# Performance work log

Measured on AMD Instinct MI355X. Metric: run time of the kernel, lower is better.

The kernel has to match this reference:

```python
import jax, jax.numpy as jnp
import numpy as np

GRAPH_RADIUS = 0.125  # gcn_cfg['graph_radius']
N, D = 4096, 256      # num samples in batch, desc_len


def setup_inputs() -> dict:
    key = jax.random.key(0)
    k1, k2, k3, k4, k5, k6 = jax.random.split(key, 6)
    centers = jax.random.uniform(k1, (N, 3), dtype=jnp.float32)  # points in unit cube
    descriptors = jax.random.normal(k2, (N, D), dtype=jnp.float32)
    # EdgeConv MLPs: torch nn.Linear(2*D, D) -> weight [D, 2*D], bias [D]
    W1 = jax.random.normal(k3, (D, 2 * D), dtype=jnp.float32) * 0.05
    b1 = jax.random.normal(k4, (D,), dtype=jnp.float32) * 0.05
    W2 = jax.random.normal(k5, (D, 2 * D), dtype=jnp.float32) * 0.05
    b2 = jax.random.normal(k6, (D,), dtype=jnp.float32) * 0.05
    return {"centers": centers, "descriptors": descriptors,
            "W1": W1, "b1": b1, "W2": W2, "b2": b2}


def reference(centers, descriptors, W1, b1, W2, b2):
    # N star graphs: graph a has edges a->k for all k != a with ||c_k - c_a|| <= r.
    # Each node k in graph a receives at most ONE message (from anchor a); the
    # anchor receives none. EdgeConv(aggr='mean') message at target i from source j
    # is mlp(cat([x_i, x_j - x_i])); mean over a single message is the message.
    n = centers.shape[0]
    d = descriptors.shape[1]
    # pairwise squared distances [N, N]
    diff = centers[:, None, :] - centers[None, :, :]
    d2 = jnp.sum(diff * diff, axis=-1)
    mask = (d2 <= GRAPH_RADIUS * GRAPH_RADIUS) & (~jnp.eye(n, dtype=bool))
    M = mask.astype(descriptors.dtype)            # M[a, k]: k is neighbor of anchor a
    deg = jnp.sum(M, axis=1, keepdims=True)       # [N, 1] neighbors per anchor

    # conv1: h1[a, k] = M[a,k] * ( cat([x_k, x_a - x_k]) @ W1^T + b1 )
    #                 = M[a,k] * ( u[k] + v[a] + b1 )
    W1a, W1b = W1[:, :d], W1[:, d:]
    u = descriptors @ (W1a - W1b).T               # target-side term  [N, D]
    v = descriptors @ W1b.T                       # anchor-side term  [N, D]

    # conv2: anchor feature h1[a, a] = 0, so message = cat([h1, -h1]) @ W2^T + b2
    #        h2[a, k] = M[a,k] * ( h1[a,k] @ (W2a - W2b)^T + b2 )
    C = (W2[:, :d] - W2[:, d:]).T                 # [D, D]

    # global_mean_pool over the N nodes of each graph a:
    # pooled[a] = (1/N) * [ (sum_k M[a,k] u[k] + deg_a*(v[a]+b1)) @ C + deg_a*b2 ]
    Mu = M @ u                                    # [N, D]
    pooled = ((Mu + deg * (v + b1)) @ C + deg * b2) / n

    return jnp.concatenate([descriptors, pooled], axis=1)  # [N, 2D]
```

## Files before the change

### kernel.cpp

```cpp
#include <hip/hip_runtime.h>

#define NPTS 4096
#define DDIM 256
#define R2V 0.015625f
#define MAXDEG 512
#define NI 4

typedef __bf16 v8bf __attribute__((ext_vector_type(8)));
typedef float v4f __attribute__((ext_vector_type(4)));
typedef unsigned short ushort_t;

static __device__ __forceinline__ float bf2f(ushort_t s) {
    union { unsigned u; float f; } w; w.u = ((unsigned)s) << 16; return w.f;
}
static __device__ __forceinline__ ushort_t f2bf(float x) {
    return __builtin_bit_cast(ushort_t, (__bf16)x);
}

__global__ void prepEFt_kernel(const float* __restrict__ W1, const float* __restrict__ W2,
                               const float* __restrict__ b1, const float* __restrict__ b2,
                               ushort_t* __restrict__ EFt, float* __restrict__ g) {
    __shared__ float cs[4][256];
    __shared__ float b1s[256];
    int l0 = blockIdx.x * 4;
    int m = threadIdx.x;
    b1s[m] = b1[m];
#pragma unroll
    for (int q = 0; q < 4; ++q)
        cs[q][m] = W2[(l0 + q) * 512 + m] - W2[(l0 + q) * 512 + 256 + m];
    __syncthreads();
    float ae[4] = {0, 0, 0, 0}, af[4] = {0, 0, 0, 0}, ag[4] = {0, 0, 0, 0};
#pragma unroll 4
    for (int k = 0; k < 256; ++k) {
        float w1a = W1[k * 512 + m];
        float w1b = W1[k * 512 + 256 + m];
        float bk = b1s[k];
#pragma unroll
        for (int q = 0; q < 4; ++q) {
            float c = cs[q][k];
            ae[q] = fmaf(w1a - w1b, c, ae[q]);
            af[q] = fmaf(w1b, c, af[q]);
            ag[q] = fmaf(bk, c, ag[q]);
        }
    }
#pragma unroll
    for (int q = 0; q < 4; ++q) {
        EFt[(l0 + q) * 256 + m] = f2bf(ae[q]);
        EFt[(256 + l0 + q) * 256 + m] = f2bf(af[q]);
        if (m == 0) g[l0 + q] = ag[q] + b2[l0 + q];
    }
}

#define BM 64
#define BN 128
__launch_bounds__(256, 1)
__global__ void gemm_kernel(const float* __restrict__ desc, const ushort_t* __restrict__ EFt,
                            ushort_t* __restrict__ PQ) {
    __shared__ ushort_t Asm[BM * 256];
    __shared__ ushort_t Bsm[BN * 256];
    int tid = threadIdx.x;
    int i0 = blockIdx.x * BM;
    int n0 = blockIdx.y * BN;
    const float* gA = desc + i0 * 256;
#pragma unroll
    for (int c = 0; c < 8; ++c) {
        int u = c * 256 + tid;
        int fb = u * 16;
        int row = fb >> 9, colb = fb & 511;
        float4 f0 = *(const float4*)(gA + u * 8);
        float4 f1 = *(const float4*)(gA + u * 8 + 4);
        ushort_t h[8];
        h[0] = f2bf(f0.x); h[1] = f2bf(f0.y); h[2] = f2bf(f0.z); h[3] = f2bf(f0.w);
        h[4] = f2bf(f1.x); h[5] = f2bf(f1.y); h[6] = f2bf(f1.z); h[7] = f2bf(f1.w);
        *(uint4*)((char*)Asm + row * 512 + (colb ^ ((row & 7) << 4))) = *(uint4*)h;
    }
    const char* gB = (const char*)(EFt + n0 * 256);
#pragma unroll
    for (int c = 0; c < 16; ++c) {
        int f = (c * 256 + tid) * 16;
        int row = f >> 9, colb = f & 511;
        uint4 v = *(const uint4*)(gB + f);
        *(uint4*)((char*)Bsm + row * 512 + (colb ^ ((row & 7) << 4))) = v;
    }
    __syncthreads();
    int w = tid >> 6, l = tid & 63;
    int mh = w >> 1, nh = w & 1;
    v4f acc[2][4] = {};
#pragma unroll
    for (int kk = 0; kk < 8; ++kk) {
        v8bf a[2], b[4];
        int kb = kk * 64 + ((l >> 4) * 16);
#pragma unroll
        for (int mi = 0; mi < 2; ++mi) {
            int r = mh * 32 + mi * 16 + (l & 15);
            a[mi] = *(const v8bf*)((const char*)Asm + r * 512 + (kb ^ ((r & 7) << 4)));
        }
#pragma unroll
        for (int ni = 0; ni < 4; ++ni) {
            int r = nh * 64 + ni * 16 + (l & 15);
            b[ni] = *(const v8bf*)((const char*)Bsm + r * 512 + (kb ^ ((r & 7) << 4)));
        }
#pragma unroll
        for (int mi = 0; mi < 2; ++mi)
#pragma unroll
            for (int ni = 0; ni < 4; ++ni)
                acc[mi][ni] = __builtin_amdgcn_mfma_f32_16x16x32_bf16(a[mi], b[ni], acc[mi][ni], 0, 0, 0);
    }
#pragma unroll
    for (int mi = 0; mi < 2; ++mi)
#pragma unroll
        for (int ni = 0; ni < 4; ++ni) {
            int rg = i0 + mh * 32 + mi * 16 + ((l >> 4) * 4);
            int cg = n0 + nh * 64 + ni * 16 + (l & 15);
#pragma unroll
            for (int j = 0; j < 4; ++j)
                PQ[(rg + j) * 512 + cg] = f2bf(acc[mi][ni][j]);
        }
}

__global__ void mask_out_kernel(const float* __restrict__ centers, const ushort_t* __restrict__ PQ,
                                const float* __restrict__ g, const float* __restrict__ desc,
                                float* __restrict__ out) {
    __shared__ int list[NI][MAXDEG];
    __shared__ int cnt[NI];
    int i0 = blockIdx.x * NI;
    int t = threadIdx.x;
    if (t < NI) cnt[t] = 0;
    __syncthreads();
    float cx[NI], cy[NI], cz[NI];
#pragma unroll
    for (int q = 0; q < NI; ++q) {
        cx[q] = centers[3 * (i0 + q)];
        cy[q] = centers[3 * (i0 + q) + 1];
        cz[q] = centers[3 * (i0 + q) + 2];
    }
    for (int j = t; j < NPTS; j += 256) {
        float px = centers[3 * j], py = centers[3 * j + 1], pz = centers[3 * j + 2];
#pragma unroll
        for (int q = 0; q < NI; ++q) {
            float dx = cx[q] - px, dy = cy[q] - py, dz = cz[q] - pz;
            float d2 = dx * dx + dy * dy + dz * dz;
            if (d2 <= R2V && j != i0 + q) {
                int p = atomicAdd(&cnt[q], 1);
                if (p < MAXDEG) list[q][p] = j;
            }
        }
    }
    __syncthreads();
    int w = t >> 6, lane = t & 63;
    int i = i0 + w;
    int n = cnt[w] < MAXDEG ? cnt[w] : MAXDEG;
    int c0 = lane * 4;
    float a0 = 0.f, a1 = 0.f, a2 = 0.f, a3 = 0.f;
    int idx = 0;
    for (; idx + 4 <= n; idx += 4) {
        int4 jj = *(const int4*)&list[w][idx];
        ushort4 r0 = *(const ushort4*)(PQ + jj.x * 512 + c0);
        ushort4 r1 = *(const ushort4*)(PQ + jj.y * 512 + c0);
        ushort4 r2 = *(const ushort4*)(PQ + jj.z * 512 + c0);
        ushort4 r3 = *(const ushort4*)(PQ + jj.w * 512 + c0);
        a0 += (bf2f(r0.x) + bf2f(r1.x)) + (bf2f(r2.x) + bf2f(r3.x));
        a1 += (bf2f(r0.y) + bf2f(r1.y)) + (bf2f(r2.y) + bf2f(r3.y));
        a2 += (bf2f(r0.z) + bf2f(r1.z)) + (bf2f(r2.z) + bf2f(r3.z));
        a3 += (bf2f(r0.w) + bf2f(r1.w)) + (bf2f(r2.w) + bf2f(r3.w));
    }
    for (; idx < n; ++idx) {
        ushort4 r = *(const ushort4*)(PQ + list[w][idx] * 512 + c0);
        a0 += bf2f(r.x); a1 += bf2f(r.y); a2 += bf2f(r.z); a3 += bf2f(r.w);
    }
    float dg = (float)cnt[w];
    ushort4 qv = *(const ushort4*)(PQ + i * 512 + 256 + c0);
    float4 gv = *(const float4*)(g + c0);
    float4 o;
    o.x = (a0 + dg * (bf2f(qv.x) + gv.x)) * (1.0f / 4096.0f);
    o.y = (a1 + dg * (bf2f(qv.y) + gv.y)) * (1.0f / 4096.0f);
    o.z = (a2 + dg * (bf2f(qv.z) + gv.z)) * (1.0f / 4096.0f);
    o.w = (a3 + dg * (bf2f(qv.w) + gv.w)) * (1.0f / 4096.0f);
    *(float4*)(out + i * 512 + 256 + c0) = o;
    *(float4*)(out + i * 512 + c0) = *(const float4*)(desc + i * 256 + c0);
}

extern "C" void kernel_launch(void* const* d_in, const int* in_sizes, int n_in,
                              void* d_out, int out_size, void* d_ws, size_t ws_size,
                              hipStream_t stream) {
    const float* centers = (const float*)d_in[0];
    const float* desc    = (const float*)d_in[1];
    const float* W1      = (const float*)d_in[2];
    const float* b1      = (const float*)d_in[3];
    const float* W2      = (const float*)d_in[4];
    const float* b2      = (const float*)d_in[5];
    float* out = (float*)d_out;

    char* ws = (char*)d_ws;
    ushort_t* EFt = (ushort_t*)(ws);
    ushort_t* PQ  = (ushort_t*)(ws + 0x40000);
    float*    g   = (float*)(ws + 0x440000);

    hipLaunchKernelGGL(prepEFt_kernel, dim3(64), dim3(256), 0, stream, W1, W2, b1, b2, EFt, g);
    hipLaunchKernelGGL(gemm_kernel, dim3(64, 4), dim3(256), 0, stream, desc, EFt, PQ);
    hipLaunchKernelGGL(mask_out_kernel, dim3(NPTS / NI), dim3(256), 0, stream, centers, PQ, g, desc, out);
}
```

Before: 49.06 us.

## Split weight-prep reduction across more blocks and batch more anchors per mask block

The weight-folding kernel now launches four times as many blocks. Each block splits the 256-long reduction over k into four partial sums, which are combined through shared memory, and a separate small reduction computes the bias term. This is meant to shorten the long serial per-thread loop that underused the GPU. The neighbor-gather kernel now processes eight anchors per block, two per wave, sharing one scan of the point centers. That trades fewer blocks for less redundant distance work.

```diff
diff --git a/kernel.cpp b/kernel.cpp
--- a/kernel.cpp
+++ b/kernel.cpp
@@ -4,7 +4,7 @@
 #define DDIM 256
 #define R2V 0.015625f
 #define MAXDEG 512
-#define NI 4
+#define NI 8
 
 typedef __bf16 v8bf __attribute__((ext_vector_type(8)));
 typedef float v4f __attribute__((ext_vector_type(4)));
@@ -21,33 +21,52 @@
                                const float* __restrict__ b1, const float* __restrict__ b2,
                                ushort_t* __restrict__ EFt, float* __restrict__ g) {
     __shared__ float cs[4][256];
-    __shared__ float b1s[256];
-    int l0 = blockIdx.x * 4;
-    int m = threadIdx.x;
-    b1s[m] = b1[m];
+    __shared__ float peA[4][4][64];
+    __shared__ float peB[4][4][64];
+    __shared__ float pg[16];
+    int b = blockIdx.x;
+    int lq = b >> 2, mq = b & 3;
+    int l0 = lq * 4;
+    int t = threadIdx.x;
+    int kq = t >> 6, ml = t & 63;
+    int m = mq * 64 + ml;
 #pragma unroll
     for (int q = 0; q < 4; ++q)
-        cs[q][m] = W2[(l0 + q) * 512 + m] - W2[(l0 + q) * 512 + 256 + m];
-    __syncthreads();
-    float ae[4] = {0, 0, 0, 0}, af[4] = {0, 0, 0, 0}, ag[4] = {0, 0, 0, 0};
+        cs[q][t] = W2[(l0 + q) * 512 + t] - W2[(l0 + q) * 512 + 256 + t];
+    __syncthreads();
+    float ae[4] = {0, 0, 0, 0}, af[4] = {0, 0, 0, 0};
+    int k0 = kq * 64;
 #pragma unroll 4
-    for (int k = 0; k < 256; ++k) {
+    for (int kk = 0; kk < 64; ++kk) {
+        int k = k0 + kk;
         float w1a = W1[k * 512 + m];
         float w1b = W1[k * 512 + 256 + m];
-        float bk = b1s[k];
+        float d = w1a - w1b;
 #pragma unroll
         for (int q = 0; q < 4; ++q) {
-            float c = cs[q][k];
-            ae[q] = fmaf(w1a - w1b, c, ae[q]);
-            af[q] = fmaf(w1b, c, af[q]);
-            ag[q] = fmaf(bk, c, ag[q]);
-        }
-    }
-#pragma unroll
-    for (int q = 0; q < 4; ++q) {
-        EFt[(l0 + q) * 256 + m] = f2bf(ae[q]);
-        EFt[(256 + l0 + q) * 256 + m] = f2bf(af[q]);
-        if (m == 0) g[l0 + q] = ag[q] + b2[l0 + q];
+            ae[q] = fmaf(d, cs[q][k], ae[q]);
+            af[q] = fmaf(w1b, cs[q][k], af[q]);
+        }
+    }
+#pragma unroll
+    for (int q = 0; q < 4; ++q) { peA[kq][q][ml] = ae[q]; peB[kq][q][ml] = af[q]; }
+    __syncthreads();
+    int q2 = t >> 6, ml2 = t & 63;
+    float sE = (peA[0][q2][ml2] + peA[1][q2][ml2]) + (peA[2][q2][ml2] + peA[3][q2][ml2]);
+    float sF = (peB[0][q2][ml2] + peB[1][q2][ml2]) + (peB[2][q2][ml2] + peB[3][q2][ml2]);
+    EFt[(l0 + q2) * 256 + mq * 64 + ml2] = f2bf(sE);
+    EFt[(256 + l0 + q2) * 256 + mq * 64 + ml2] = f2bf(sF);
+    if (mq == 0) {
+        if (t < 16) {
+            int q = t >> 2, kqq = t & 3;
+            float s = 0.f;
+            for (int kk = 0; kk < 64; ++kk)
+                s = fmaf(b1[kqq * 64 + kk], cs[q][kqq * 64 + kk], s);
+            pg[t] = s;
+        }
+        __syncthreads();
+        if (t < 4)
+            g[l0 + t] = ((pg[t * 4] + pg[t * 4 + 1]) + (pg[t * 4 + 2] + pg[t * 4 + 3])) + b2[l0 + t];
     }
 }
 
@@ -148,36 +167,40 @@
     }
     __syncthreads();
     int w = t >> 6, lane = t & 63;
-    int i = i0 + w;
-    int n = cnt[w] < MAXDEG ? cnt[w] : MAXDEG;
     int c0 = lane * 4;
-    float a0 = 0.f, a1 = 0.f, a2 = 0.f, a3 = 0.f;
-    int idx = 0;
-    for (; idx + 4 <= n; idx += 4) {
-        int4 jj = *(const int4*)&list[w][idx];
-        ushort4 r0 = *(const ushort4*)(PQ + jj.x * 512 + c0);
-        ushort4 r1 = *(const ushort4*)(PQ + jj.y * 512 + c0);
-        ushort4 r2 = *(const ushort4*)(PQ + jj.z * 512 + c0);
-        ushort4 r3 = *(const ushort4*)(PQ + jj.w * 512 + c0);
-        a0 += (bf2f(r0.x) + bf2f(r1.x)) + (bf2f(r2.x) + bf2f(r3.x));
-        a1 += (bf2f(r0.y) + bf2f(r1.y)) + (bf2f(r2.y) + bf2f(r3.y));
-        a2 += (bf2f(r0.z) + bf2f(r1.z)) + (bf2f(r2.z) + bf2f(r3.z));
-        a3 += (bf2f(r0.w) + bf2f(r1.w)) + (bf2f(r2.w) + bf2f(r3.w));
-    }
-    for (; idx < n; ++idx) {
-        ushort4 r = *(const ushort4*)(PQ + list[w][idx] * 512 + c0);
-        a0 += bf2f(r.x); a1 += bf2f(r.y); a2 += bf2f(r.z); a3 += bf2f(r.w);
-    }
-    float dg = (float)cnt[w];
-    ushort4 qv = *(const ushort4*)(PQ + i * 512 + 256 + c0);
-    float4 gv = *(const float4*)(g + c0);
-    float4 o;
-    o.x = (a0 + dg * (bf2f(qv.x) + gv.x)) * (1.0f / 4096.0f);
-    o.y = (a1 + dg * (bf2f(qv.y) + gv.y)) * (1.0f / 4096.0f);
-    o.z = (a2 + dg * (bf2f(qv.z) + gv.z)) * (1.0f / 4096.0f);
-    o.w = (a3 + dg * (bf2f(qv.w) + gv.w)) * (1.0f / 4096.0f);
-    *(float4*)(out + i * 512 + 256 + c0) = o;
-    *(float4*)(out + i * 512 + c0) = *(const float4*)(desc + i * 256 + c0);
+#pragma unroll
+    for (int s = 0; s < 2; ++s) {
+        int q = w * 2 + s;
+        int i = i0 + q;
+        int n = cnt[q] < MAXDEG ? cnt[q] : MAXDEG;
+        float a0 = 0.f, a1 = 0.f, a2 = 0.f, a3 = 0.f;
+        int idx = 0;
+        for (; idx + 4 <= n; idx += 4) {
+            int4 jj = *(const int4*)&list[q][idx];
+            ushort4 r0 = *(const ushort4*)(PQ + jj.x * 512 + c0);
+            ushort4 r1 = *(const ushort4*)(PQ + jj.y * 512 + c0);
+            ushort4 r2 = *(const ushort4*)(PQ + jj.z * 512 + c0);
+            ushort4 r3 = *(const ushort4*)(PQ + jj.w * 512 + c0);
+            a0 += (bf2f(r0.x) + bf2f(r1.x)) + (bf2f(r2.x) + bf2f(r3.x));
+            a1 += (bf2f(r0.y) + bf2f(r1.y)) + (bf2f(r2.y) + bf2f(r3.y));
+            a2 += (bf2f(r0.z) + bf2f(r1.z)) + (bf2f(r2.z) + bf2f(r3.z));
+            a3 += (bf2f(r0.w) + bf2f(r1.w)) + (bf2f(r2.w) + bf2f(r3.w));
+        }
+        for (; idx < n; ++idx) {
+            ushort4 r = *(const ushort4*)(PQ + list[q][idx] * 512 + c0);
+            a0 += bf2f(r.x); a1 += bf2f(r.y); a2 += bf2f(r.z); a3 += bf2f(r.w);
+        }
+        float dg = (float)cnt[q];
+        ushort4 qv = *(const ushort4*)(PQ + i * 512 + 256 + c0);
+        float4 gv = *(const float4*)(g + c0);
+        float4 o;
+        o.x = (a0 + dg * (bf2f(qv.x) + gv.x)) * (1.0f / 4096.0f);
+        o.y = (a1 + dg * (bf2f(qv.y) + gv.y)) * (1.0f / 4096.0f);
+        o.z = (a2 + dg * (bf2f(qv.z) + gv.z)) * (1.0f / 4096.0f);
+        o.w = (a3 + dg * (bf2f(qv.w) + gv.w)) * (1.0f / 4096.0f);
+        *(float4*)(out + i * 512 + 256 + c0) = o;
+        *(float4*)(out + i * 512 + c0) = *(const float4*)(desc + i * 256 + c0);
+    }
 }
 
 extern "C" void kernel_launch(void* const* d_in, const int* in_sizes, int n_in,
@@ -196,7 +219,7 @@
     ushort_t* PQ  = (ushort_t*)(ws + 0x40000);
     float*    g   = (float*)(ws + 0x440000);
 
-    hipLaunchKernelGGL(prepEFt_kernel, dim3(64), dim3(256), 0, stream, W1, W2, b1, b2, EFt, g);
+    hipLaunchKernelGGL(prepEFt_kernel, dim3(256), dim3(256), 0, stream, W1, W2, b1, b2, EFt, g);
     hipLaunchKernelGGL(gemm_kernel, dim3(64, 4), dim3(256), 0, stream, desc, EFt, PQ);
     hipLaunchKernelGGL(mask_out_kernel, dim3(NPTS / NI), dim3(256), 0, stream, centers, PQ, g, desc, out);
 }
```

After: 42.16 us. 1.16x faster.
